# Optimization experiments

Measured on AMD Instinct MI355X. Metric: run time of the kernel, lower is better.

The kernel has to match this reference:

```python
import jax, jax.numpy as jnp
import numpy as np

B, L, D_MODEL, H = 4, 2048, 1024, 16
HD = D_MODEL // H  # head_dim = 64


def _rope_tables(seq_len, dim, dtype):
    inv_freq = 1.0 / (10000.0 ** (jnp.arange(0, dim, 2, dtype=jnp.float32) / dim))
    t = jnp.arange(seq_len, dtype=jnp.float32)
    freqs = jnp.outer(t, inv_freq)  # (S, dim/2)
    return jnp.cos(freqs).astype(dtype), jnp.sin(freqs).astype(dtype)


def _apply_rope(x):
    # x: (B, H, S, d)
    cos, sin = _rope_tables(x.shape[-2], x.shape[-1], x.dtype)  # (S, d/2)
    x_even = x[..., 0::2]
    x_odd = x[..., 1::2]
    out_even = x_even * cos - x_odd * sin
    out_odd = x_even * sin + x_odd * cos
    return jnp.stack([out_even, out_odd], axis=-1).reshape(x.shape)


def setup_inputs() -> dict:
    key = jax.random.key(0)
    ks = jax.random.split(key, 9)
    s = 1.0 / np.sqrt(D_MODEL)
    inp = {
        "query": jax.random.normal(ks[0], (B, L, D_MODEL), dtype=jnp.float32),
        "Wq": jax.random.uniform(ks[1], (D_MODEL, D_MODEL), jnp.float32, -s, s),
        "bq": jax.random.uniform(ks[2], (D_MODEL,), jnp.float32, -s, s),
        "Wk": jax.random.uniform(ks[3], (D_MODEL, D_MODEL), jnp.float32, -s, s),
        "bk": jax.random.uniform(ks[4], (D_MODEL,), jnp.float32, -s, s),
        "Wv": jax.random.uniform(ks[5], (D_MODEL, D_MODEL), jnp.float32, -s, s),
        "bv": jax.random.uniform(ks[6], (D_MODEL,), jnp.float32, -s, s),
        "Wo": jax.random.uniform(ks[7], (D_MODEL, D_MODEL), jnp.float32, -s, s),
        "bo": jax.random.uniform(ks[8], (D_MODEL,), jnp.float32, -s, s),
    }
    return inp


def reference(query, Wq, bq, Wk, bk, Wv, bv, Wo, bo):
    Bq, Lq, _ = query.shape
    # projections (torch Linear: x @ W.T + b), split into heads -> (B, H, L, d)
    def proj(x, W, b):
        y = x @ W.T + b
        return y.reshape(Bq, Lq, H, HD).transpose(0, 2, 1, 3)
    q = _apply_rope(proj(query, Wq, bq))
    k = _apply_rope(proj(query, Wk, bk))
    v = proj(query, Wv, bv)
    scores = jnp.einsum("bhqd,bhkd->bhqk", q, k) / np.sqrt(HD)
    causal_mask = jnp.triu(jnp.ones((Lq, Lq), dtype=bool), k=1)
    scores = jnp.where(causal_mask[None, None, :, :], -jnp.inf, scores)
    attn = jax.nn.softmax(scores, axis=-1)
    out = jnp.einsum("bhqk,bhkd->bhqd", attn, v)
    out = out.transpose(0, 2, 1, 3).reshape(Bq, Lq, D_MODEL)
    return out @ Wo.T + bo
```

## Files before the change

### kernel.cpp

```cpp
#include <hip/hip_runtime.h>
#include <hip/hip_bf16.h>
#include <math.h>

#define L_SEQ  2048
#define DMODEL 1024
#define NHEAD  16
#define HEADD  64

typedef __attribute__((ext_vector_type(8))) short short8;
typedef __attribute__((ext_vector_type(4))) short short4v;
typedef __attribute__((ext_vector_type(4))) float f32x4;

#define LDA 32

static __device__ __forceinline__ unsigned short f2bf(float f) {
    unsigned int u = __float_as_uint(f);
    unsigned int r = (u + 0x7fffu + ((u >> 16) & 1u)) >> 16;
    return (unsigned short)r;
}

static __device__ __forceinline__ void dma16(const unsigned short* g, unsigned short* l) {
    __builtin_amdgcn_global_load_lds((const __attribute__((address_space(1))) void*)g,
                                     (__attribute__((address_space(3))) void*)l, 16, 0, 0);
}

__global__ void cvt_f32_bf16(const float* __restrict__ in,
                             unsigned short* __restrict__ out, int n4) {
    int i = blockIdx.x * blockDim.x + threadIdx.x;
    if (i >= n4) return;
    float4 v = reinterpret_cast<const float4*>(in)[i];
    ushort4 o;
    o.x = f2bf(v.x); o.y = f2bf(v.y); o.z = f2bf(v.z); o.w = f2bf(v.w);
    reinterpret_cast<ushort4*>(out)[i] = o;
}

__global__ void cvt_weights(const float* __restrict__ Wq, const float* __restrict__ Wk,
                            const float* __restrict__ Wv, const float* __restrict__ Wo,
                            unsigned short* __restrict__ dst) {
    int i = blockIdx.x * blockDim.x + threadIdx.x;
    int which = i >> 18;
    const float* src = which == 0 ? Wq : which == 1 ? Wk : which == 2 ? Wv : Wo;
    float4 v = reinterpret_cast<const float4*>(src)[i & 262143];
    ushort4 o;
    o.x = f2bf(v.x); o.y = f2bf(v.y); o.z = f2bf(v.z); o.w = f2bf(v.w);
    reinterpret_cast<ushort4*>(dst)[i] = o;
}

__global__ void build_rope(float* __restrict__ tab) {
    int i = blockIdx.x * blockDim.x + threadIdx.x;
    int lpos = i >> 5, i2 = i & 31;
    float inv_f = expf(-0.28782313662425574f * (float)i2);
    float ang = (float)lpos * inv_f;
    tab[2 * i]     = cosf(ang);
    tab[2 * i + 1] = sinf(ang);
}

#define BKP 32

__global__ __launch_bounds__(256) void proj_qkv(
    const unsigned short* __restrict__ X,
    const unsigned short* __restrict__ Wqkv,
    const float* __restrict__ bq_,
    const float* __restrict__ bk_,
    const float* __restrict__ bv_,
    const float* __restrict__ rope,
    unsigned short* __restrict__ Qb,
    unsigned short* __restrict__ Kb,
    unsigned short* __restrict__ Vr)
{
    __shared__ unsigned short a_lds[3][128 * BKP];
    __shared__ unsigned short b_lds[3][128 * BKP];

    const int tid  = threadIdx.x;
    const int lane = tid & 63;
    const int w    = tid >> 6;
    const int wm   = w & 1, wn = w >> 1;
    const int quad = lane >> 4, l16 = lane & 15;

    const int orig = blockIdx.y * 24 + blockIdx.x;
    const int swz  = (orig & 7) * 192 + (orig >> 3);
    const int bx   = swz % 24;
    const int by   = swz / 24;
    const int m0   = by * 128;
    const int n0   = bx * 128;

    const int sel = bx >> 3;
    const float* bias   = sel == 0 ? bq_ : (sel == 1 ? bk_ : bv_);
    unsigned short* out = sel == 0 ? Qb  : (sel == 1 ? Kb  : Vr);

    const int st_row = lane >> 2;
    const int st_col = (((lane & 3) ^ ((lane >> 3) & 3)) << 3);
    const int rd = ((quad ^ ((l16 >> 1) & 3)) << 3);

    f32x4 acc[4][4];
#pragma unroll
    for (int i = 0; i < 4; ++i)
#pragma unroll
        for (int j = 0; j < 4; ++j) acc[i][j] = (f32x4){0.f, 0.f, 0.f, 0.f};

    const unsigned short* Xs = X    + (size_t)(m0 + w * 32 + st_row) * DMODEL + st_col;
    const unsigned short* Ws = Wqkv + (size_t)(n0 + w * 32 + st_row) * DMODEL + st_col;
    const int ldsA0 = (w * 32) * BKP, ldsA1 = (w * 32 + 16) * BKP;

#pragma unroll
    for (int p = 0; p < 2; ++p) {
        const int kk = p * BKP;
        dma16(Xs + kk,               &a_lds[p][ldsA0]);
        dma16(Xs + 16 * DMODEL + kk, &a_lds[p][ldsA1]);
        dma16(Ws + kk,               &b_lds[p][ldsA0]);
        dma16(Ws + 16 * DMODEL + kk, &b_lds[p][ldsA1]);
    }
    asm volatile("s_waitcnt vmcnt(4)" ::: "memory");
    __builtin_amdgcn_s_barrier();

    for (int kt = 0; kt < 32; ++kt) {
        const int slot = kt % 3;
        const int ps   = (kt + 2) % 3;
        const int kk   = ((kt + 2) & 31) * BKP;

        short8 af[4], bf[2];
#pragma unroll
        for (int i = 0; i < 4; ++i)
            af[i] = *reinterpret_cast<const short8*>(
                &a_lds[slot][(wm * 64 + i * 16 + l16) * BKP + rd]);
#pragma unroll
        for (int j = 0; j < 2; ++j)
            bf[j] = *reinterpret_cast<const short8*>(
                &b_lds[slot][(wn * 64 + j * 16 + l16) * BKP + rd]);
        dma16(Xs + kk,               &a_lds[ps][ldsA0]);
        dma16(Xs + 16 * DMODEL + kk, &a_lds[ps][ldsA1]);
        __builtin_amdgcn_s_barrier();
        asm volatile("s_waitcnt lgkmcnt(0)" ::: "memory");
        __builtin_amdgcn_sched_barrier(0);
        __builtin_amdgcn_s_setprio(1);
#pragma unroll
        for (int i = 0; i < 4; ++i)
#pragma unroll
            for (int j = 0; j < 2; ++j)
                acc[i][j] = __builtin_amdgcn_mfma_f32_16x16x32_bf16(af[i], bf[j], acc[i][j], 0, 0, 0);
        __builtin_amdgcn_s_setprio(0);
        __builtin_amdgcn_s_barrier();

#pragma unroll
        for (int j = 0; j < 2; ++j)
            bf[j] = *reinterpret_cast<const short8*>(
                &b_lds[slot][(wn * 64 + (2 + j) * 16 + l16) * BKP + rd]);
        dma16(Ws + kk,               &b_lds[ps][ldsA0]);
        dma16(Ws + 16 * DMODEL + kk, &b_lds[ps][ldsA1]);
        __builtin_amdgcn_s_barrier();
        asm volatile("s_waitcnt lgkmcnt(0)" ::: "memory");
        __builtin_amdgcn_sched_barrier(0);
        __builtin_amdgcn_s_setprio(1);
#pragma unroll
        for (int i = 0; i < 4; ++i)
#pragma unroll
            for (int j = 0; j < 2; ++j)
                acc[i][2 + j] = __builtin_amdgcn_mfma_f32_16x16x32_bf16(af[i], bf[j], acc[i][2 + j], 0, 0, 0);
        __builtin_amdgcn_s_setprio(0);
        asm volatile("s_waitcnt vmcnt(4)" ::: "memory");
        __builtin_amdgcn_s_barrier();
    }
    asm volatile("s_waitcnt vmcnt(0)" ::: "memory");

#pragma unroll
    for (int jf = 0; jf < 4; ++jf) {
        int nn = (bx & 7) * 128 + wn * 64 + jf * 16 + l16;
        float bval = bias[nn];
        int d  = nn & (HEADD - 1);
        int h  = nn >> 6;
        float sgn = (d & 1) ? 1.0f : -1.0f;
        int i2 = d >> 1;
#pragma unroll
        for (int mf = 0; mf < 4; ++mf) {
#pragma unroll
            for (int r = 0; r < 4; ++r) {
                int m_g = m0 + wm * 64 + mf * 16 + quad * 4 + r;
                float v = acc[mf][jf][r] + bval;
                int b    = m_g >> 11;
                int lpos = m_g & (L_SEQ - 1);
                if (sel < 2) {
                    float p = __shfl_xor(v, 1);
                    float2 cs = *reinterpret_cast<const float2*>(&rope[(size_t)(lpos * 32 + i2) * 2]);
                    v = v * cs.x + sgn * cs.y * p;
                    if (sel == 0) v *= 0.18033688011112042f;
                }
                out[((size_t)(b * NHEAD + h) * L_SEQ + lpos) * HEADD + d] = f2bf(v);
            }
        }
    }
}

__global__ __launch_bounds__(256) void transpose_v(
    const unsigned short* __restrict__ Vr, unsigned short* __restrict__ Vt)
{
    __shared__ unsigned short tile[64 * 72];
    const int tid = threadIdx.x;
    const int bh  = blockIdx.y;
    const int l0  = blockIdx.x * 64;
#pragma unroll
    for (int t = 0; t < 2; ++t) {
        int c = tid + t * 256;
        int row = c >> 3, cc = (c & 7) << 3;
        int4 v = *reinterpret_cast<const int4*>(Vr + ((size_t)bh * L_SEQ + l0 + row) * HEADD + cc);
        *reinterpret_cast<int4*>(&tile[row * 72 + cc]) = v;
    }
    __syncthreads();
#pragma unroll
    for (int t = 0; t < 2; ++t) {
        int c = tid + t * 256;
        int d = c >> 3, lc = (c & 7) << 3;
        union { unsigned short u[8]; int4 v; } tt;
#pragma unroll
        for (int j = 0; j < 8; ++j) tt.u[j] = tile[(lc + j) * 72 + d];
        *reinterpret_cast<int4*>(Vt + ((size_t)bh * HEADD + d) * L_SEQ + l0 + lc) = tt.v;
    }
}

#define LDK 88

__global__ __launch_bounds__(256) void attn_fwd(
    const unsigned short* __restrict__ Q,
    const unsigned short* __restrict__ K,
    const unsigned short* __restrict__ Vt,
    unsigned short* __restrict__ Oa)
{
    __shared__ unsigned short k_lds[64 * LDK];
    __shared__ unsigned short v_lds[64 * LDK];
    const int tid  = threadIdx.x;
    const int lane = tid & 63;
    const int w    = tid >> 6;
    const int quad = lane >> 4, l16 = lane & 15;
    const int pair = blockIdx.y;
    const int bh   = blockIdx.x;
    const size_t base = (size_t)bh * L_SEQ * HEADD;

    const int srow0 = tid >> 3;
    const int scc   = (tid & 7) << 3;
    const int b = bh >> 4, h = bh & 15;

    for (int half = 0; half < 2; ++half) {
        const int qb = half ? (31 - pair) : pair;
        const int qrow = qb * 64 + w * 16 + l16;

        short8 qf[2];
#pragma unroll
        for (int ks = 0; ks < 2; ++ks)
            qf[ks] = *reinterpret_cast<const short8*>(Q + base + (size_t)qrow * HEADD + ks * 32 + quad * 8);

        f32x4 o[4];
#pragma unroll
        for (int nt = 0; nt < 4; ++nt) o[nt] = (f32x4){0.f, 0.f, 0.f, 0.f};
        float lsum = 0.f;

        int4 ka0 = *reinterpret_cast<const int4*>(K  + base + (size_t)srow0 * HEADD + scc);
        int4 ka1 = *reinterpret_cast<const int4*>(K  + base + (size_t)(srow0 + 32) * HEADD + scc);
        int4 va0 = *reinterpret_cast<const int4*>(Vt + base + (size_t)srow0 * L_SEQ + scc);
        int4 va1 = *reinterpret_cast<const int4*>(Vt + base + (size_t)(srow0 + 32) * L_SEQ + scc);

        for (int kb = 0; kb <= qb; ++kb) {
            __syncthreads();
            *reinterpret_cast<int4*>(&k_lds[srow0 * LDK + scc])        = ka0;
            *reinterpret_cast<int4*>(&k_lds[(srow0 + 32) * LDK + scc]) = ka1;
            *reinterpret_cast<int4*>(&v_lds[srow0 * LDK + scc])        = va0;
            *reinterpret_cast<int4*>(&v_lds[(srow0 + 32) * LDK + scc]) = va1;
            __syncthreads();

            if (kb < qb) {
                int kn = kb + 1;
                ka0 = *reinterpret_cast<const int4*>(K  + base + (size_t)(kn * 64 + srow0) * HEADD + scc);
                ka1 = *reinterpret_cast<const int4*>(K  + base + (size_t)(kn * 64 + srow0 + 32) * HEADD + scc);
                va0 = *reinterpret_cast<const int4*>(Vt + base + (size_t)srow0 * L_SEQ + kn * 64 + scc);
                va1 = *reinterpret_cast<const int4*>(Vt + base + (size_t)(srow0 + 32) * L_SEQ + kn * 64 + scc);
            }

            f32x4 st[4];
#pragma unroll
            for (int nt = 0; nt < 4; ++nt) st[nt] = (f32x4){0.f, 0.f, 0.f, 0.f};
            __builtin_amdgcn_s_setprio(1);
#pragma unroll
            for (int ks = 0; ks < 2; ++ks)
#pragma unroll
                for (int nt = 0; nt < 4; ++nt) {
                    short8 kf = *reinterpret_cast<const short8*>(&k_lds[(nt * 16 + l16) * LDK + ks * 32 + quad * 8]);
                    st[nt] = __builtin_amdgcn_mfma_f32_16x16x32_bf16(kf, qf[ks], st[nt], 0, 0, 0);
                }
            __builtin_amdgcn_s_setprio(0);

            if (kb == qb) {
#pragma unroll
                for (int nt = 0; nt < 4; ++nt)
#pragma unroll
                    for (int r = 0; r < 4; ++r) {
                        int seqcol = kb * 64 + nt * 16 + quad * 4 + r;
                        if (seqcol > qrow) st[nt][r] = -INFINITY;
                    }
            }

            short4v pfrag[4];
#pragma unroll
            for (int nt = 0; nt < 4; ++nt) {
                float p0 = __builtin_amdgcn_exp2f(st[nt][0]);
                float p1 = __builtin_amdgcn_exp2f(st[nt][1]);
                float p2 = __builtin_amdgcn_exp2f(st[nt][2]);
                float p3 = __builtin_amdgcn_exp2f(st[nt][3]);
                lsum += (p0 + p1) + (p2 + p3);
                unsigned u0 = __float_as_uint(p0) + 0x8000u;
                unsigned u1 = __float_as_uint(p1) + 0x8000u;
                unsigned u2 = __float_as_uint(p2) + 0x8000u;
                unsigned u3 = __float_as_uint(p3) + 0x8000u;
                union { unsigned u[2]; short4v v; } pk;
                pk.u[0] = (u0 >> 16) | (u1 & 0xffff0000u);
                pk.u[1] = (u2 >> 16) | (u3 & 0xffff0000u);
                pfrag[nt] = pk.v;
            }

            __builtin_amdgcn_s_setprio(1);
#pragma unroll
            for (int c = 0; c < 4; ++c)
#pragma unroll
                for (int nt2 = 0; nt2 < 4; ++nt2) {
                    short4v vf = *reinterpret_cast<const short4v*>(
                        &v_lds[(nt2 * 16 + l16) * LDK + c * 16 + quad * 4]);
                    o[nt2] = __builtin_amdgcn_mfma_f32_16x16x16bf16_1k(pfrag[c], vf, o[nt2], 0, 0, 0);
                }
            __builtin_amdgcn_s_setprio(0);
        }

        lsum += __shfl_xor(lsum, 16);
        lsum += __shfl_xor(lsum, 32);
        float rs[4];
#pragma unroll
        for (int r = 0; r < 4; ++r) rs[r] = __shfl(lsum, quad * 4 + r);
#pragma unroll
        for (int r = 0; r < 4; ++r) {
            float inv = 1.0f / rs[r];
            int lg = qb * 64 + w * 16 + quad * 4 + r;
#pragma unroll
            for (int nt = 0; nt < 4; ++nt) {
                int d = nt * 16 + l16;
                Oa[(size_t)(b * L_SEQ + lg) * DMODEL + h * HEADD + d] = f2bf(o[nt][r] * inv);
            }
        }
    }
}

__global__ __launch_bounds__(256) void out_gemm(
    const unsigned short* __restrict__ X,
    const unsigned short* __restrict__ W,
    const float* __restrict__ bias,
    float* __restrict__ out)
{
    __shared__ unsigned short a_lds[3][128 * BKP];
    __shared__ unsigned short b_lds[3][128 * BKP];
    const int tid  = threadIdx.x;
    const int lane = tid & 63;
    const int w    = tid >> 6;
    const int wm   = w & 1, wn = w >> 1;
    const int quad = lane >> 4, l16 = lane & 15;

    const int orig = blockIdx.y * 8 + blockIdx.x;
    const int swz  = (orig & 7) * 64 + (orig >> 3);
    const int m0 = (swz >> 3) * 128;
    const int n0 = (swz & 7) * 128;

    const int st_row = lane >> 2;
    const int st_col = (((lane & 3) ^ ((lane >> 3) & 3)) << 3);
    const int rd = ((quad ^ ((l16 >> 1) & 3)) << 3);

    f32x4 acc[4][4];
#pragma unroll
    for (int i = 0; i < 4; ++i)
#pragma unroll
        for (int j = 0; j < 4; ++j) acc[i][j] = (f32x4){0.f, 0.f, 0.f, 0.f};

    const unsigned short* Xs = X + (size_t)(m0 + w * 32 + st_row) * DMODEL + st_col;
    const unsigned short* Ws = W + (size_t)(n0 + w * 32 + st_row) * DMODEL + st_col;
    const int ldsA0 = (w * 32) * BKP, ldsA1 = (w * 32 + 16) * BKP;

#pragma unroll
    for (int p = 0; p < 2; ++p) {
        const int kk = p * BKP;
        dma16(Xs + kk,               &a_lds[p][ldsA0]);
        dma16(Xs + 16 * DMODEL + kk, &a_lds[p][ldsA1]);
        dma16(Ws + kk,               &b_lds[p][ldsA0]);
        dma16(Ws + 16 * DMODEL + kk, &b_lds[p][ldsA1]);
    }
    asm volatile("s_waitcnt vmcnt(4)" ::: "memory");
    __builtin_amdgcn_s_barrier();

    for (int kt = 0; kt < 32; ++kt) {
        const int slot = kt % 3;
        const int ps   = (kt + 2) % 3;
        const int kk   = ((kt + 2) & 31) * BKP;

        dma16(Xs + kk,               &a_lds[ps][ldsA0]);
        dma16(Xs + 16 * DMODEL + kk, &a_lds[ps][ldsA1]);
        dma16(Ws + kk,               &b_lds[ps][ldsA0]);
        dma16(Ws + 16 * DMODEL + kk, &b_lds[ps][ldsA1]);

        short8 af[4], bf[4];
#pragma unroll
        for (int i = 0; i < 4; ++i)
            af[i] = *reinterpret_cast<const short8*>(
                &a_lds[slot][(wm * 64 + i * 16 + l16) * BKP + rd]);
#pragma unroll
        for (int j = 0; j < 4; ++j)
            bf[j] = *reinterpret_cast<const short8*>(
                &b_lds[slot][(wn * 64 + j * 16 + l16) * BKP + rd]);
        asm volatile("s_waitcnt lgkmcnt(0)" ::: "memory");
        __builtin_amdgcn_sched_barrier(0);
        __builtin_amdgcn_s_setprio(1);
#pragma unroll
        for (int i = 0; i < 4; ++i)
#pragma unroll
            for (int j = 0; j < 4; ++j)
                acc[i][j] = __builtin_amdgcn_mfma_f32_16x16x32_bf16(af[i], bf[j], acc[i][j], 0, 0, 0);
        __builtin_amdgcn_s_setprio(0);
        asm volatile("s_waitcnt vmcnt(4)" ::: "memory");
        __builtin_amdgcn_s_barrier();
    }
    asm volatile("s_waitcnt vmcnt(0)" ::: "memory");

#pragma unroll
    for (int nt = 0; nt < 4; ++nt) {
        int n_g = n0 + wn * 64 + nt * 16 + l16;
        float bv = bias[n_g];
#pragma unroll
        for (int mt = 0; mt < 4; ++mt)
#pragma unroll
            for (int r = 0; r < 4; ++r) {
                int m_g = m0 + wm * 64 + mt * 16 + quad * 4 + r;
                out[(size_t)m_g * DMODEL + n_g] = acc[mt][nt][r] + bv;
            }
    }
}

extern "C" void kernel_launch(void* const* d_in, const int* in_sizes, int n_in,
                              void* d_out, int out_size, void* d_ws, size_t ws_size,
                              hipStream_t stream) {
    const float* query = (const float*)d_in[0];
    const float* Wq = (const float*)d_in[1];
    const float* bq = (const float*)d_in[2];
    const float* Wk = (const float*)d_in[3];
    const float* bk = (const float*)d_in[4];
    const float* Wv = (const float*)d_in[5];
    const float* bv = (const float*)d_in[6];
    const float* Wo = (const float*)d_in[7];
    const float* bo = (const float*)d_in[8];
    float* out = (float*)d_out;

    unsigned short* ws  = (unsigned short*)d_ws;
    unsigned short* xb  = ws;
    unsigned short* wqb = xb  + (size_t)8388608;
    unsigned short* wkb = wqb + 1048576;
    unsigned short* wvb = wkb + 1048576;
    unsigned short* wob = wvb + 1048576;
    unsigned short* Qb  = wob + 1048576;
    unsigned short* Kb  = Qb  + 8388608;
    unsigned short* Vr  = Kb  + 8388608;
    unsigned short* Vtb = Vr  + 8388608;
    unsigned short* Ab  = Vtb + 8388608;
    float* rope = (float*)(Ab + 8388608);

    (void)wkb; (void)wvb;

    build_rope<<<256, 256, 0, stream>>>(rope);
    cvt_f32_bf16<<<8192, 256, 0, stream>>>(query, xb, 2097152);
    cvt_weights<<<4096, 256, 0, stream>>>(Wq, Wk, Wv, Wo, wqb);

    proj_qkv<<<dim3(24, 64), 256, 0, stream>>>(xb, wqb, bq, bk, bv, rope, Qb, Kb, Vr);
    transpose_v<<<dim3(32, 64), 256, 0, stream>>>(Vr, Vtb);
    attn_fwd<<<dim3(64, 16), 256, 0, stream>>>(Qb, Kb, Vtb, Ab);
    out_gemm<<<dim3(8, 64), 256, 0, stream>>>(Ab, wob, bo, out);
}
```

Before: 305.4 us.

## Double-buffer K/V tiles via direct global-to-LDS DMA with XOR swizzle

Replaces register-staged K/V loads with global_load_lds DMA into double-buffered shared memory, so the next tile streams into LDS while the current tile is computed. One barrier per iteration replaces two. Padded rows give way to an XOR-swizzled 64-wide layout to avoid bank conflicts. The cost is twice the LDS footprint, a redundant prefetch on the last iteration, and a full vmcnt wait each step.

Result: faster. 295.7 us (-3.2%).

```diff
diff --git a/kernel.cpp b/kernel.cpp
--- a/kernel.cpp
+++ b/kernel.cpp
@@ -216,16 +216,14 @@
     }
 }
 
-#define LDK 88
-
 __global__ __launch_bounds__(256) void attn_fwd(
     const unsigned short* __restrict__ Q,
     const unsigned short* __restrict__ K,
     const unsigned short* __restrict__ Vt,
     unsigned short* __restrict__ Oa)
 {
-    __shared__ unsigned short k_lds[64 * LDK];
-    __shared__ unsigned short v_lds[64 * LDK];
+    __shared__ unsigned short k_lds[2][64 * 64];
+    __shared__ unsigned short v_lds[2][64 * 64];
     const int tid  = threadIdx.x;
     const int lane = tid & 63;
     const int w    = tid >> 6;
@@ -233,10 +231,16 @@
     const int pair = blockIdx.y;
     const int bh   = blockIdx.x;
     const size_t base = (size_t)bh * L_SEQ * HEADD;
-
-    const int srow0 = tid >> 3;
-    const int scc   = (tid & 7) << 3;
     const int b = bh >> 4, h = bh & 15;
+
+    const int srow  = lane >> 3;
+    const int sslot = lane & 7;
+    const int ssw   = ((sslot ^ srow) << 3);
+    const unsigned short* Ksrc = K  + base + (size_t)(w * 8 + srow) * HEADD  + ssw;
+    const unsigned short* Vsrc = Vt + base + (size_t)(w * 8 + srow) * L_SEQ + ssw;
+    const int d0 = (w * 8) * 64;
+    const int d1 = (32 + w * 8) * 64;
+    const int swr = (l16 & 7);
 
     for (int half = 0; half < 2; ++half) {
         const int qb = half ? (31 - pair) : pair;
@@ -252,26 +256,21 @@
         for (int nt = 0; nt < 4; ++nt) o[nt] = (f32x4){0.f, 0.f, 0.f, 0.f};
         float lsum = 0.f;
 
-        int4 ka0 = *reinterpret_cast<const int4*>(K  + base + (size_t)srow0 * HEADD + scc);
-        int4 ka1 = *reinterpret_cast<const int4*>(K  + base + (size_t)(srow0 + 32) * HEADD + scc);
-        int4 va0 = *reinterpret_cast<const int4*>(Vt + base + (size_t)srow0 * L_SEQ + scc);
-        int4 va1 = *reinterpret_cast<const int4*>(Vt + base + (size_t)(srow0 + 32) * L_SEQ + scc);
-
+        dma16(Ksrc,                 &k_lds[0][d0]);
+        dma16(Ksrc + 32 * HEADD,    &k_lds[0][d1]);
+        dma16(Vsrc,                 &v_lds[0][d0]);
+        dma16(Vsrc + 32 * L_SEQ,    &v_lds[0][d1]);
+        asm volatile("s_waitcnt vmcnt(0)" ::: "memory");
+        __builtin_amdgcn_s_barrier();
+
+        int cur = 0;
         for (int kb = 0; kb <= qb; ++kb) {
-            __syncthreads();
-            *reinterpret_cast<int4*>(&k_lds[srow0 * LDK + scc])        = ka0;
-            *reinterpret_cast<int4*>(&k_lds[(srow0 + 32) * LDK + scc]) = ka1;
-            *reinterpret_cast<int4*>(&v_lds[srow0 * LDK + scc])        = va0;
-            *reinterpret_cast<int4*>(&v_lds[(srow0 + 32) * LDK + scc]) = va1;
-            __syncthreads();
-
-            if (kb < qb) {
-                int kn = kb + 1;
-                ka0 = *reinterpret_cast<const int4*>(K  + base + (size_t)(kn * 64 + srow0) * HEADD + scc);
-                ka1 = *reinterpret_cast<const int4*>(K  + base + (size_t)(kn * 64 + srow0 + 32) * HEADD + scc);
-                va0 = *reinterpret_cast<const int4*>(Vt + base + (size_t)srow0 * L_SEQ + kn * 64 + scc);
-                va1 = *reinterpret_cast<const int4*>(Vt + base + (size_t)(srow0 + 32) * L_SEQ + kn * 64 + scc);
-            }
+            const int kn = (kb + 1) <= qb ? (kb + 1) : 0;
+            const int nb = cur ^ 1;
+            dma16(Ksrc + (size_t)(kn * 64) * HEADD,        &k_lds[nb][d0]);
+            dma16(Ksrc + (size_t)(kn * 64 + 32) * HEADD,   &k_lds[nb][d1]);
+            dma16(Vsrc + kn * 64,                          &v_lds[nb][d0]);
+            dma16(Vsrc + kn * 64 + 32 * L_SEQ,             &v_lds[nb][d1]);
 
             f32x4 st[4];
 #pragma unroll
@@ -281,7 +280,8 @@
             for (int ks = 0; ks < 2; ++ks)
 #pragma unroll
                 for (int nt = 0; nt < 4; ++nt) {
-                    short8 kf = *reinterpret_cast<const short8*>(&k_lds[(nt * 16 + l16) * LDK + ks * 32 + quad * 8]);
+                    short8 kf = *reinterpret_cast<const short8*>(
+                        &k_lds[cur][(nt * 16 + l16) * 64 + (((ks * 4 + quad) ^ swr) << 3)]);
                     st[nt] = __builtin_amdgcn_mfma_f32_16x16x32_bf16(kf, qf[ks], st[nt], 0, 0, 0);
                 }
             __builtin_amdgcn_s_setprio(0);
@@ -320,10 +320,15 @@
 #pragma unroll
                 for (int nt2 = 0; nt2 < 4; ++nt2) {
                     short4v vf = *reinterpret_cast<const short4v*>(
-                        &v_lds[(nt2 * 16 + l16) * LDK + c * 16 + quad * 4]);
+                        &v_lds[cur][(nt2 * 16 + l16) * 64 +
+                                    (((c * 2 + (quad >> 1)) ^ swr) << 3) + ((quad & 1) << 2)]);
                     o[nt2] = __builtin_amdgcn_mfma_f32_16x16x16bf16_1k(pfrag[c], vf, o[nt2], 0, 0, 0);
                 }
             __builtin_amdgcn_s_setprio(0);
+
+            asm volatile("s_waitcnt vmcnt(0)" ::: "memory");
+            __builtin_amdgcn_s_barrier();
+            cur ^= 1;
         }
 
         lsum += __shfl_xor(lsum, 16);
```
